# Kernel tuning notes

Measured on AMD Instinct MI355X. Metric: run time of the kernel, lower is better.

## Reference

```python
import jax, jax.numpy as jnp
import numpy as np

N_GENES = 4264
IN_DIM = 1613
N_REL = 4
DIM1, DIM2, DIM3 = 1340, 920, 740
N_DRUGS = 4000
N_EDGES = 100000
N_NODES = N_DRUGS + N_GENES


def setup_inputs() -> dict:
    key = jax.random.key(0)
    ks = jax.random.split(key, 16)
    inp = {}
    inp["x"] = jax.random.normal(ks[0], (N_DRUGS, IN_DIM), dtype=jnp.float32)
    inp["gene_emb"] = jax.random.normal(ks[1], (N_GENES, IN_DIM), dtype=jnp.float32)
    s = 0.02
    inp["w_rel1"] = jax.random.normal(ks[2], (N_REL, IN_DIM, DIM1), dtype=jnp.float32) * s
    inp["root1"] = jax.random.normal(ks[3], (IN_DIM, DIM1), dtype=jnp.float32) * s
    inp["b1"] = jnp.zeros((DIM1,), dtype=jnp.float32)
    inp["w_rel2"] = jax.random.normal(ks[4], (N_REL, DIM1, DIM2), dtype=jnp.float32) * s
    inp["root2"] = jax.random.normal(ks[5], (DIM1, DIM2), dtype=jnp.float32) * s
    inp["b2"] = jnp.zeros((DIM2,), dtype=jnp.float32)
    inp["lin1_w"] = jax.random.normal(ks[6], (DIM2, DIM3), dtype=jnp.float32) * s
    inp["lin1_b"] = jnp.zeros((DIM3,), dtype=jnp.float32)
    inp["lin2_w"] = jax.random.normal(ks[7], (DIM3, 2), dtype=jnp.float32) * s
    inp["lin2_b"] = jnp.zeros((2,), dtype=jnp.float32)
    inp["edge_index"] = jax.random.randint(ks[8], (2, N_EDGES), 0, N_NODES, dtype=jnp.int32)
    inp["edge_type"] = jax.random.randint(ks[9], (N_EDGES,), 0, N_REL, dtype=jnp.int32)
    return inp


def rgcn_conv(x, edge_index, edge_type, w_rel, root, bias):
    # PyG RGCNConv: per-relation linear transform of source node features,
    # scatter-MEAN aggregation per (target node, relation), plus root + bias.
    # Transform-then-gather (N << E) is mathematically identical to gather-then-transform.
    n = x.shape[0]
    r = w_rel.shape[0]
    h = jnp.einsum('nf,rfo->rno', x, w_rel)          # (R, N, out)
    src, dst = edge_index[0], edge_index[1]
    msg = h[edge_type, src]                           # (E, out) gathered messages
    seg = dst * r + edge_type                         # fused (node, relation) segment id
    sums = jax.ops.segment_sum(msg, seg, num_segments=n * r)
    cnts = jax.ops.segment_sum(jnp.ones_like(msg[:, 0]), seg, num_segments=n * r)
    mean = sums / jnp.maximum(cnts, 1.0)[:, None]
    agg = mean.reshape(n, r, -1).sum(axis=1)          # sum over relations
    return agg + x @ root + bias


def reference(x, gene_emb, w_rel1, root1, b1, w_rel2, root2, b2,
              lin1_w, lin1_b, lin2_w, lin2_b, edge_index, edge_type):
    # eval mode: dropout is identity
    xf = jnp.concatenate([x, gene_emb], axis=0)       # (N, 1613)
    h = jax.nn.relu(rgcn_conv(xf, edge_index, edge_type, w_rel1, root1, b1))
    h = jax.nn.relu(rgcn_conv(h, edge_index, edge_type, w_rel2, root2, b2))
    emb = jax.nn.relu(h @ lin1_w + lin1_b)            # (N, 740)
    logits = emb @ lin2_w + lin2_b                    # (N, 2)
    return jax.nn.log_softmax(logits, axis=-1), emb
```

## Files before the change

### kernel.cpp

```cpp
#include <hip/hip_runtime.h>
#include <math.h>

#define N_DRUGS 4000
#define NN      8264
#define IN_DIM  1613
#define NRELS   4
#define DD1     1340
#define DD2     920
#define DD3     740
#define NEDGE   100000
#define NSEG    (NN * NRELS)

#define K1P     1632
#define K2P     1344
#define K3P     928
#define N1PAD   1408
#define N2PAD   1024
#define N3PAD   768
#define MT      65

typedef unsigned short u16;
typedef __attribute__((ext_vector_type(8))) short short8;
typedef __attribute__((ext_vector_type(4))) short short4v;
typedef __attribute__((ext_vector_type(4))) float floatx4;

__device__ __forceinline__ u16 f2bf(float f) {
  union { float f; unsigned u; } v; v.f = f;
  unsigned u = v.u + 0x7fffu + ((v.u >> 16) & 1u);
  return (u16)(u >> 16);
}
__device__ __forceinline__ float bf2f(u16 h) {
  union { unsigned u; float f; } v; v.u = ((unsigned)h) << 16;
  return v.f;
}

__device__ __forceinline__ void gload16(const u16* g, u16* l) {
  __builtin_amdgcn_global_load_lds(
      (const __attribute__((address_space(1))) unsigned int*)g,
      (__attribute__((address_space(3))) unsigned int*)l, 16, 0, 0);
}

__global__ void k_zero_i32(int* p, int n) {
  int i = blockIdx.x * 256 + threadIdx.x;
  if (i < n) p[i] = 0;
}

__global__ void k_zero_u16v(u16* p, long long nvec) {
  long long i = (long long)blockIdx.x * 256 + threadIdx.x;
  if (i < nvec) {
    short8 z = {0,0,0,0,0,0,0,0};
    *((short8*)p + i) = z;
  }
}

__global__ void k_copy_i32(const int* a, int* b, int n) {
  int i = blockIdx.x * 256 + threadIdx.x;
  if (i < n) b[i] = a[i];
}

__global__ void k_hist(const int* __restrict__ ei, const int* __restrict__ et,
                       int* __restrict__ counts) {
  int e = blockIdx.x * 256 + threadIdx.x;
  if (e < NEDGE) {
    int dst = ei[NEDGE + e];
    atomicAdd(&counts[dst * 4 + et[e]], 1);
  }
}

__global__ void k_scan(const int* __restrict__ counts, int* __restrict__ offsets) {
  __shared__ int part[1024];
  int tid = threadIdx.x;
  const int chunk = (NSEG + 1023) / 1024;
  int lo = tid * chunk, hi = min(lo + chunk, NSEG);
  int s = 0;
  for (int i = lo; i < hi; i++) s += counts[i];
  part[tid] = s;
  __syncthreads();
  for (int off = 1; off < 1024; off <<= 1) {
    int v = (tid >= off) ? part[tid - off] : 0;
    __syncthreads();
    part[tid] += v;
    __syncthreads();
  }
  int base = (tid == 0) ? 0 : part[tid - 1];
  for (int i = lo; i < hi; i++) { offsets[i] = base; base += counts[i]; }
  if (tid == 0) offsets[NSEG] = part[1023];
}

__global__ void k_fill(const int* __restrict__ ei, const int* __restrict__ et,
                       int* __restrict__ cursors, int* __restrict__ ssrc) {
  int e = blockIdx.x * 256 + threadIdx.x;
  if (e < NEDGE) {
    int src = ei[e], dst = ei[NEDGE + e];
    int pos = atomicAdd(&cursors[dst * 4 + et[e]], 1);
    if (pos < NEDGE) ssrc[pos] = src;
  }
}

__global__ void k_build_xf(const float* __restrict__ x, const float* __restrict__ gene,
                           u16* __restrict__ xf) {
  int n = blockIdx.x;
  const float* srow = (n < N_DRUGS) ? (x + (long long)n * IN_DIM)
                                    : (gene + (long long)(n - N_DRUGS) * IN_DIM);
  u16* dst = xf + (long long)n * K1P;
  for (int f = threadIdx.x; f < K1P; f += 256)
    dst[f] = (f < IN_DIM) ? f2bf(srow[f]) : (u16)0;
}

__global__ void k_transpose(const float* __restrict__ in, int K, int N,
                            u16* __restrict__ out, int ldd,
                            long long strideIn, long long strideOut) {
  __shared__ float t[32][33];
  const float* inp = in + (long long)blockIdx.z * strideIn;
  u16* outp = out + (long long)blockIdx.z * strideOut;
  int k0 = blockIdx.x * 32, n0 = blockIdx.y * 32;
  int tx = threadIdx.x, ty = threadIdx.y;
  for (int i = ty; i < 32; i += 8) {
    int k = k0 + i, n = n0 + tx;
    t[i][tx] = (k < K && n < N) ? inp[(long long)k * N + n] : 0.f;
  }
  __syncthreads();
  for (int i = ty; i < 32; i += 8) {
    int n = n0 + i, k = k0 + tx;
    if (n < N && k < K) outp[(long long)n * ldd + k] = f2bf(t[tx][i]);
  }
}

__global__ void k_agg2(const u16* __restrict__ T, int ldT, int slotOfs,
                       u16* __restrict__ HACC, int ldH, int F,
                       const int* __restrict__ offsets, const int* __restrict__ ssrc,
                       int rbase, int init) {
  int node = blockIdx.x;
  int s0 = node * 4 + rbase;
  int b0 = offsets[s0],     e0 = offsets[s0 + 1];
  int b1 = offsets[s0 + 1], e1 = offsets[s0 + 2];
  float inv0 = (e0 > b0) ? 1.0f / (float)(e0 - b0) : 0.0f;
  float inv1 = (e1 > b1) ? 1.0f / (float)(e1 - b1) : 0.0f;
  u16* o = HACC + (long long)node * ldH;
  int F8 = F >> 3;
  for (int f8 = threadIdx.x; f8 < F8; f8 += 256) {
    int fo = f8 << 3;
    float a0=0.f,a1=0.f,a2=0.f,a3=0.f,a4=0.f,a5=0.f,a6=0.f,a7=0.f;
    for (int e = b0; e < e0; e++) {
      short8 v = *(const short8*)(T + (long long)ssrc[e] * ldT + fo);
      a0 += bf2f((u16)v[0]); a1 += bf2f((u16)v[1]);
      a2 += bf2f((u16)v[2]); a3 += bf2f((u16)v[3]);
      a4 += bf2f((u16)v[4]); a5 += bf2f((u16)v[5]);
      a6 += bf2f((u16)v[6]); a7 += bf2f((u16)v[7]);
    }
    float c0=0.f,c1=0.f,c2=0.f,c3=0.f,c4=0.f,c5=0.f,c6=0.f,c7=0.f;
    for (int e = b1; e < e1; e++) {
      short8 v = *(const short8*)(T + (long long)ssrc[e] * ldT + slotOfs + fo);
      c0 += bf2f((u16)v[0]); c1 += bf2f((u16)v[1]);
      c2 += bf2f((u16)v[2]); c3 += bf2f((u16)v[3]);
      c4 += bf2f((u16)v[4]); c5 += bf2f((u16)v[5]);
      c6 += bf2f((u16)v[6]); c7 += bf2f((u16)v[7]);
    }
    float r0 = a0*inv0 + c0*inv1, r1 = a1*inv0 + c1*inv1;
    float r2 = a2*inv0 + c2*inv1, r3 = a3*inv0 + c3*inv1;
    float r4 = a4*inv0 + c4*inv1, r5 = a5*inv0 + c5*inv1;
    float r6 = a6*inv0 + c6*inv1, r7 = a7*inv0 + c7*inv1;
    if (!init) {
      short8 pv = *(const short8*)(o + fo);
      r0 += bf2f((u16)pv[0]); r1 += bf2f((u16)pv[1]);
      r2 += bf2f((u16)pv[2]); r3 += bf2f((u16)pv[3]);
      r4 += bf2f((u16)pv[4]); r5 += bf2f((u16)pv[5]);
      r6 += bf2f((u16)pv[6]); r7 += bf2f((u16)pv[7]);
    }
    short8 ov;
    ov[0] = (short)f2bf(r0); ov[1] = (short)f2bf(r1);
    ov[2] = (short)f2bf(r2); ov[3] = (short)f2bf(r3);
    ov[4] = (short)f2bf(r4); ov[5] = (short)f2bf(r5);
    ov[6] = (short)f2bf(r6); ov[7] = (short)f2bf(r7);
    *(short8*)(o + fo) = ov;
  }
  if ((F & 7) && threadIdx.x == 0) {
    for (int f = F & ~7; f < F; f++) {
      float a = 0.f, c = 0.f;
      for (int e = b0; e < e0; e++) a += bf2f(T[(long long)ssrc[e] * ldT + f]);
      for (int e = b1; e < e1; e++) c += bf2f(T[(long long)ssrc[e] * ldT + slotOfs + f]);
      float r = a * inv0 + c * inv1;
      if (!init) r += bf2f(o[f]);
      o[f] = f2bf(r);
    }
  }
}

#define TBUF (128 * 32)

__global__ __launch_bounds__(256)
void k_gemm3(const u16* __restrict__ A, int lda,
             const u16* __restrict__ B, int ldb, int ksteps,
             void* __restrict__ Cout, int ldc,
             const u16* __restrict__ Cacc, int ldacc,
             int nreal, int nlimit, int mlimit,
             const float* __restrict__ bias, int relu, int f32out,
             int mtiles, int ntiles)
{
  int f = blockIdx.x;
  int xr = f & 7, q = f >> 3;
  int Ma = (mtiles + 7) >> 3;
  int ncol = q / Ma;
  int mi = ((q - ncol * Ma) << 3) + xr;
  if (mi >= mtiles) return;

  __shared__ __align__(16) u16 At[3 * TBUF];
  __shared__ __align__(16) u16 Bt[3 * TBUF];
  int tid = threadIdx.x;
  int wave = tid >> 6, lane = tid & 63;
  int wm = (wave >> 1) << 6, wn = (wave & 1) << 6;
  int qd = lane >> 4, l16 = lane & 15;

  const u16* Ag = A + (long long)mi * 128 * lda;
  const u16* Bg = B + (long long)ncol * 128 * ldb;

  int row = tid >> 2, cc = tid & 3;
  int swc = cc ^ ((row >> 1) & 3);
  const u16* gA0 = Ag + (long long)row * lda + swc * 8;
  const u16* gA1 = Ag + (long long)(row + 64) * lda + swc * 8;
  const u16* gB0 = Bg + (long long)row * ldb + swc * 8;
  const u16* gB1 = Bg + (long long)(row + 64) * ldb + swc * 8;
  int d0 = tid * 8;
  int d1 = tid * 8 + 64 * 32;
  int rofs = ((qd ^ ((l16 >> 1) & 3)) << 3);

  unsigned baseA = (unsigned)(unsigned long long)(void*)At;
  unsigned baseB = (unsigned)(unsigned long long)(void*)Bt;
  unsigned offA[4], offB[4];
#pragma unroll
  for (int i = 0; i < 4; i++) {
    offA[i] = (unsigned)(((wm + i * 16 + l16) * 32 + rofs) * 2);
    offB[i] = (unsigned)(((wn + i * 16 + l16) * 32 + rofs) * 2);
  }

  gload16(gA0, At + d0); gload16(gA1, At + d1);
  gload16(gB0, Bt + d0); gload16(gB1, Bt + d1);
  if (ksteps > 1) {
    gload16(gA0 + 32, At + TBUF + d0); gload16(gA1 + 32, At + TBUF + d1);
    gload16(gB0 + 32, Bt + TBUF + d0); gload16(gB1 + 32, Bt + TBUF + d1);
  }

  floatx4 acc[4][4] = {};
  int bs = 0;

  for (int ks = 0; ks < ksteps; ks++) {
    if (ks + 1 < ksteps) asm volatile("s_waitcnt vmcnt(4)" ::: "memory");
    else                 asm volatile("s_waitcnt vmcnt(0)" ::: "memory");
    __builtin_amdgcn_s_barrier();
    __builtin_amdgcn_sched_barrier(0);
    if (ks + 2 < ksteps) {
      int ns = bs + 2; if (ns >= 3) ns -= 3;
      int kb = (ks + 2) * 32;
      u16* An = At + ns * TBUF;
      u16* Bn = Bt + ns * TBUF;
      gload16(gA0 + kb, An + d0); gload16(gA1 + kb, An + d1);
      gload16(gB0 + kb, Bn + d0); gload16(gB1 + kb, Bn + d1);
    }
    unsigned sb = (unsigned)(bs * (TBUF * 2));
    short8 af[4], bfr[4];
#pragma unroll
    for (int i = 0; i < 4; i++)
      asm volatile("ds_read_b128 %0, %1" : "=v"(af[i]) : "v"(baseA + sb + offA[i]));
#pragma unroll
    for (int j = 0; j < 4; j++)
      asm volatile("ds_read_b128 %0, %1" : "=v"(bfr[j]) : "v"(baseB + sb + offB[j]));
    asm volatile("s_waitcnt lgkmcnt(0)" ::: "memory");
    __builtin_amdgcn_sched_barrier(0);
#pragma unroll
    for (int i = 0; i < 4; i++)
#pragma unroll
      for (int j = 0; j < 4; j++)
        acc[i][j] = __builtin_amdgcn_mfma_f32_16x16x32_bf16(af[i], bfr[j], acc[i][j], 0, 0, 0);
    bs++; if (bs >= 3) bs = 0;
  }

#pragma unroll
  for (int i = 0; i < 4; i++) {
#pragma unroll
    for (int j = 0; j < 4; j++) {
      int col = ncol * 128 + wn + j * 16 + l16;
      if (col >= nlimit) continue;
      float bv = (bias && col < nreal) ? bias[col] : 0.f;
#pragma unroll
      for (int rg = 0; rg < 4; rg++) {
        int rowc = mi * 128 + wm + i * 16 + qd * 4 + rg;
        if (rowc >= mlimit) continue;
        float v = 0.f;
        if (col < nreal) {
          v = acc[i][j][rg] + bv;
          if (Cacc) v += bf2f(Cacc[(long long)rowc * ldacc + col]);
          if (relu) v = fmaxf(v, 0.f);
        }
        if (f32out) ((float*)Cout)[(long long)rowc * ldc + col] = v;
        else        ((u16*)Cout)[(long long)rowc * ldc + col] = f2bf(v);
      }
    }
  }
}

__global__ __launch_bounds__(256)
void k_gemm4(const u16* __restrict__ A, int lda,
             const u16* __restrict__ B, int ldb, int ksteps,
             void* __restrict__ Cout, int ldc,
             const u16* __restrict__ Cacc, int ldacc,
             int nreal, int nlimit, int mlimit,
             const float* __restrict__ bias, int relu, int f32out,
             int mtiles, int ntiles)
{
  int f = blockIdx.x;
  int xr = f & 7, q = f >> 3;
  int Ma = (mtiles + 7) >> 3;
  int ncol = q / Ma;
  int mi = ((q - ncol * Ma) << 3) + xr;
  if (mi >= mtiles) return;

  __shared__ __align__(16) u16 At[4 * TBUF];
  __shared__ __align__(16) u16 Bt[4 * TBUF];
  int tid = threadIdx.x;
  int wave = tid >> 6, lane = tid & 63;
  int wm = (wave >> 1) << 6, wn = (wave & 1) << 6;
  int qd = lane >> 4, l16 = lane & 15;

  const u16* Ag = A + (long long)mi * 128 * lda;
  const u16* Bg = B + (long long)ncol * 128 * ldb;

  int row = tid >> 2, cc = tid & 3;
  int swc = cc ^ ((row >> 1) & 3);
  const u16* gA0 = Ag + (long long)row * lda + swc * 8;
  const u16* gA1 = Ag + (long long)(row + 64) * lda + swc * 8;
  const u16* gB0 = Bg + (long long)row * ldb + swc * 8;
  const u16* gB1 = Bg + (long long)(row + 64) * ldb + swc * 8;
  int d0 = tid * 8;
  int d1 = tid * 8 + 64 * 32;
  int rofs = ((qd ^ ((l16 >> 1) & 3)) << 3);

  unsigned baseA = (unsigned)(unsigned long long)(void*)At;
  unsigned baseB = (unsigned)(unsigned long long)(void*)Bt;
  unsigned offA[4], offB[4];
#pragma unroll
  for (int i = 0; i < 4; i++) {
    offA[i] = (unsigned)(((wm + i * 16 + l16) * 32 + rofs) * 2);
    offB[i] = (unsigned)(((wn + i * 16 + l16) * 32 + rofs) * 2);
  }

  gload16(gA0, At + d0); gload16(gA1, At + d1);
  gload16(gB0, Bt + d0); gload16(gB1, Bt + d1);
  if (ksteps > 1) {
    gload16(gA0 + 32, At + TBUF + d0); gload16(gA1 + 32, At + TBUF + d1);
    gload16(gB0 + 32, Bt + TBUF + d0); gload16(gB1 + 32, Bt + TBUF + d1);
  }
  if (ksteps > 2) {
    gload16(gA0 + 64, At + 2 * TBUF + d0); gload16(gA1 + 64, At + 2 * TBUF + d1);
    gload16(gB0 + 64, Bt + 2 * TBUF + d0); gload16(gB1 + 64, Bt + 2 * TBUF + d1);
  }

  floatx4 acc[4][4] = {};
  int bs = 0;

  for (int ks = 0; ks < ksteps; ks++) {
    int rem = ksteps - 1 - ks;
    if (rem >= 2)      asm volatile("s_waitcnt vmcnt(8)" ::: "memory");
    else if (rem == 1) asm volatile("s_waitcnt vmcnt(4)" ::: "memory");
    else               asm volatile("s_waitcnt vmcnt(0)" ::: "memory");
    __builtin_amdgcn_s_barrier();
    __builtin_amdgcn_sched_barrier(0);
    if (ks + 3 < ksteps) {
      int ns = (bs + 3) & 3;
      int kb = (ks + 3) * 32;
      u16* An = At + ns * TBUF;
      u16* Bn = Bt + ns * TBUF;
      gload16(gA0 + kb, An + d0); gload16(gA1 + kb, An + d1);
      gload16(gB0 + kb, Bn + d0); gload16(gB1 + kb, Bn + d1);
    }
    unsigned sb = (unsigned)(bs * (TBUF * 2));
    short8 af[4], bfr[4];
#pragma unroll
    for (int i = 0; i < 4; i++)
      asm volatile("ds_read_b128 %0, %1" : "=v"(af[i]) : "v"(baseA + sb + offA[i]));
#pragma unroll
    for (int j = 0; j < 4; j++)
      asm volatile("ds_read_b128 %0, %1" : "=v"(bfr[j]) : "v"(baseB + sb + offB[j]));
    asm volatile("s_waitcnt lgkmcnt(0)" ::: "memory");
    __builtin_amdgcn_sched_barrier(0);
#pragma unroll
    for (int i = 0; i < 4; i++)
#pragma unroll
      for (int j = 0; j < 4; j++)
        acc[i][j] = __builtin_amdgcn_mfma_f32_16x16x32_bf16(af[i], bfr[j], acc[i][j], 0, 0, 0);
    bs = (bs + 1) & 3;
  }

#pragma unroll
  for (int i = 0; i < 4; i++) {
#pragma unroll
    for (int j = 0; j < 4; j++) {
      int col = ncol * 128 + wn + j * 16 + l16;
      if (col >= nlimit) continue;
      float bv = (bias && col < nreal) ? bias[col] : 0.f;
#pragma unroll
      for (int rg = 0; rg < 4; rg++) {
        int rowc = mi * 128 + wm + i * 16 + qd * 4 + rg;
        if (rowc >= mlimit) continue;
        float v = 0.f;
        if (col < nreal) {
          v = acc[i][j][rg] + bv;
          if (Cacc) v += bf2f(Cacc[(long long)rowc * ldacc + col]);
          if (relu) v = fmaxf(v, 0.f);
        }
        if (f32out) ((float*)Cout)[(long long)rowc * ldc + col] = v;
        else        ((u16*)Cout)[(long long)rowc * ldc + col] = f2bf(v);
      }
    }
  }
}

__global__ void k_lin2(const float* __restrict__ emb, const float* __restrict__ w,
                       const float* __restrict__ b, float* __restrict__ out) {
  int node = blockIdx.x * 4 + (threadIdx.x >> 6);
  int lane = threadIdx.x & 63;
  if (node >= NN) return;
  const float* e = emb + (long long)node * DD3;
  float a0 = 0.f, a1 = 0.f;
  for (int f = lane; f < DD3; f += 64) {
    float v = e[f];
    a0 += v * w[2 * f];
    a1 += v * w[2 * f + 1];
  }
  for (int off = 32; off > 0; off >>= 1) {
    a0 += __shfl_down(a0, off);
    a1 += __shfl_down(a1, off);
  }
  if (lane == 0) {
    a0 += b[0]; a1 += b[1];
    float m = fmaxf(a0, a1);
    float ls = m + logf(expf(a0 - m) + expf(a1 - m));
    out[(long long)node * 2]     = a0 - ls;
    out[(long long)node * 2 + 1] = a1 - ls;
  }
}

extern "C" void kernel_launch(void* const* d_in, const int* in_sizes, int n_in,
                              void* d_out, int out_size, void* d_ws, size_t ws_size,
                              hipStream_t stream)
{
  const float* x      = (const float*)d_in[0];
  const float* gene   = (const float*)d_in[1];
  const float* w_rel1 = (const float*)d_in[2];
  const float* root1  = (const float*)d_in[3];
  const float* b1     = (const float*)d_in[4];
  const float* w_rel2 = (const float*)d_in[5];
  const float* root2  = (const float*)d_in[6];
  const float* b2     = (const float*)d_in[7];
  const float* lin1_w = (const float*)d_in[8];
  const float* lin1_b = (const float*)d_in[9];
  const float* lin2_w = (const float*)d_in[10];
  const float* lin2_b = (const float*)d_in[11];
  const int*   ei     = (const int*)d_in[12];
  const int*   et     = (const int*)d_in[13];
  float* out = (float*)d_out;

  char* ws = (char*)d_ws;
  size_t off = 0;
  auto alloc = [&](size_t bytes) -> void* {
    void* p = ws + off;
    off += (bytes + 255) & ~(size_t)255;
    return p;
  };
  const size_t W1SLOT = (size_t)N1PAD * K1P;
  const size_t W2SLOT = (size_t)N2PAD * K2P;
  u16* XF   = (u16*)alloc((size_t)NN * K1P * 2);
  u16* T    = (u16*)alloc((size_t)NN * 2 * N1PAD * 2);
  u16* HACC = (u16*)alloc((size_t)NN * K2P * 2);
  u16* H1   = (u16*)alloc((size_t)NN * K2P * 2);
  u16* W1P  = (u16*)alloc(2 * W1SLOT * 2);
  u16* W1R  = (u16*)alloc(W1SLOT * 2);
  u16* W2P  = (u16*)alloc(2 * W2SLOT * 2);
  u16* W2R  = (u16*)alloc(W2SLOT * 2);
  u16* W3T  = (u16*)alloc((size_t)N3PAD * K3P * 2);
  int* counts  = (int*)alloc((NSEG + 1) * 4);
  int* offsets = (int*)alloc((NSEG + 1) * 4);
  int* ssrc    = (int*)alloc((size_t)NEDGE * 4);
  u16* H2 = XF;
  float* emb = out + 2 * NN;

  if (off > ws_size) return;

  k_zero_i32<<<(NSEG + 1 + 255) / 256, 256, 0, stream>>>(counts, NSEG + 1);
  k_hist<<<(NEDGE + 255) / 256, 256, 0, stream>>>(ei, et, counts);
  k_scan<<<1, 1024, 0, stream>>>(counts, offsets);
  k_copy_i32<<<(NSEG + 255) / 256, 256, 0, stream>>>(offsets, counts, NSEG);
  k_fill<<<(NEDGE + 255) / 256, 256, 0, stream>>>(ei, et, counts, ssrc);

  long long wtot = 3LL * W1SLOT + 3LL * W2SLOT + (long long)N3PAD * K3P;
  k_zero_u16v<<<(unsigned)((wtot / 8 + 255) / 256), 256, 0, stream>>>(W1P, wtot / 8);
  dim3 tb(32, 8);
  dim3 g_t1((IN_DIM + 31) / 32, (DD1 + 31) / 32, 2);
  dim3 g_t1s((IN_DIM + 31) / 32, (DD1 + 31) / 32, 1);
  dim3 g_t2((DD1 + 31) / 32, (DD2 + 31) / 32, 2);
  dim3 g_t2s((DD1 + 31) / 32, (DD2 + 31) / 32, 1);

  k_build_xf<<<NN, 256, 0, stream>>>(x, gene, XF);

  const int Ma8 = 8 * ((MT + 7) / 8);
  const int gP1 = Ma8 * (2 * N1PAD / 128);
  const int gR1 = Ma8 * (N1PAD / 128);
  const int gP2 = Ma8 * (2 * N2PAD / 128);
  const int gR2 = Ma8 * (N2PAD / 128);
  const int gL3 = Ma8 * (N3PAD / 128);

  k_transpose<<<g_t1, tb, 0, stream>>>(w_rel1, IN_DIM, DD1, W1P, K1P,
                                       (long long)IN_DIM * DD1, (long long)W1SLOT);
  k_gemm4<<<gP1, 256, 0, stream>>>(XF, K1P, W1P, K1P, K1P / 32,
      T, 2 * N1PAD, (const u16*)nullptr, 0, 2 * N1PAD, 2 * N1PAD, NN,
      (const float*)nullptr, 0, 0, MT, 2 * N1PAD / 128);
  k_agg2<<<NN, 256, 0, stream>>>(T, 2 * N1PAD, N1PAD, HACC, K2P, DD1, offsets, ssrc, 0, 1);
  k_transpose<<<g_t1, tb, 0, stream>>>(w_rel1 + 2LL * IN_DIM * DD1, IN_DIM, DD1, W1P, K1P,
                                       (long long)IN_DIM * DD1, (long long)W1SLOT);
  k_gemm3<<<gP1, 256, 0, stream>>>(XF, K1P, W1P, K1P, K1P / 32,
      T, 2 * N1PAD, (const u16*)nullptr, 0, 2 * N1PAD, 2 * N1PAD, NN,
      (const float*)nullptr, 0, 0, MT, 2 * N1PAD / 128);
  k_agg2<<<NN, 256, 0, stream>>>(T, 2 * N1PAD, N1PAD, HACC, K2P, DD1, offsets, ssrc, 2, 0);
  k_transpose<<<g_t1s, tb, 0, stream>>>(root1, IN_DIM, DD1, W1R, K1P, 0, 0);
  k_gemm3<<<gR1, 256, 0, stream>>>(XF, K1P, W1R, K1P, K1P / 32,
      H1, K2P, HACC, K2P, DD1, K2P, NN, b1, 1, 0, MT, N1PAD / 128);

  k_transpose<<<g_t2, tb, 0, stream>>>(w_rel2, DD1, DD2, W2P, K2P,
                                       (long long)DD1 * DD2, (long long)W2SLOT);
  k_gemm3<<<gP2, 256, 0, stream>>>(H1, K2P, W2P, K2P, K2P / 32,
      T, 2 * N2PAD, (const u16*)nullptr, 0, 2 * N2PAD, 2 * N2PAD, NN,
      (const float*)nullptr, 0, 0, MT, 2 * N2PAD / 128);
  k_agg2<<<NN, 256, 0, stream>>>(T, 2 * N2PAD, N2PAD, HACC, K3P, DD2, offsets, ssrc, 0, 1);
  k_transpose<<<g_t2, tb, 0, stream>>>(w_rel2 + 2LL * DD1 * DD2, DD1, DD2, W2P, K2P,
                                       (long long)DD1 * DD2, (long long)W2SLOT);
  k_gemm3<<<gP2, 256, 0, stream>>>(H1, K2P, W2P, K2P, K2P / 32,
      T, 2 * N2PAD, (const u16*)nullptr, 0, 2 * N2PAD, 2 * N2PAD, NN,
      (const float*)nullptr, 0, 0, MT, 2 * N2PAD / 128);
  k_agg2<<<NN, 256, 0, stream>>>(T, 2 * N2PAD, N2PAD, HACC, K3P, DD2, offsets, ssrc, 2, 0);
  k_transpose<<<g_t2s, tb, 0, stream>>>(root2, DD1, DD2, W2R, K2P, 0, 0);
  k_gemm3<<<gR2, 256, 0, stream>>>(H1, K2P, W2R, K2P, K2P / 32,
      H2, K3P, HACC, K3P, DD2, K3P, NN, b2, 1, 0, MT, N2PAD / 128);

  k_transpose<<<dim3((DD2 + 31) / 32, (DD3 + 31) / 32, 1), tb, 0, stream>>>(
      lin1_w, DD2, DD3, W3T, K3P, 0, 0);
  k_gemm3<<<gL3, 256, 0, stream>>>(H2, K3P, W3T, K3P, K3P / 32,
      emb, DD3, (const u16*)nullptr, 0, DD3, DD3, NN, lin1_b, 1, 1, MT, N3PAD / 128);

  k_lin2<<<(NN + 3) / 4, 256, 0, stream>>>(emb, lin2_w, lin2_b, out);
}
```

Measured before the change: 1.001 ms.

## Use wider 128x256 tile GEMM with 512 threads for relation-pair transforms

Replaces the 128x128 four-stage gemm4 and the 128x128 gemm3 calls for the per-relation-pair transforms with a new k_gemmW kernel. It uses 8 waves per block, a 128x256 output tile and a three-stage LDS pipeline, and its epilogue is simplified to a plain bf16 store. The wider tile reuses each A tile across twice as many output columns, which halves A global loads and block count per GEMM. In exchange, LDS use per block grows and there are fewer blocks, which could reduce occupancy or leave CUs idle in the tail.

```diff
diff --git a/kernel.cpp b/kernel.cpp
--- a/kernel.cpp
+++ b/kernel.cpp
@@ -21,7 +21,6 @@
 
 typedef unsigned short u16;
 typedef __attribute__((ext_vector_type(8))) short short8;
-typedef __attribute__((ext_vector_type(4))) short short4v;
 typedef __attribute__((ext_vector_type(4))) float floatx4;
 
 __device__ __forceinline__ u16 f2bf(float f) {
@@ -187,6 +186,8 @@
 }
 
 #define TBUF (128 * 32)
+#define ATBW (128 * 32)
+#define BTBW (256 * 32)
 
 __global__ __launch_bounds__(256)
 void k_gemm3(const u16* __restrict__ A, int lda,
@@ -298,14 +299,12 @@
   }
 }
 
-__global__ __launch_bounds__(256)
-void k_gemm4(const u16* __restrict__ A, int lda,
+__global__ __launch_bounds__(512)
+void k_gemmW(const u16* __restrict__ A, int lda,
              const u16* __restrict__ B, int ldb, int ksteps,
              void* __restrict__ Cout, int ldc,
-             const u16* __restrict__ Cacc, int ldacc,
-             int nreal, int nlimit, int mlimit,
-             const float* __restrict__ bias, int relu, int f32out,
-             int mtiles, int ntiles)
+             int nlimit, int mlimit,
+             int mtiles)
 {
   int f = blockIdx.x;
   int xr = f & 7, q = f >> 3;
@@ -314,26 +313,32 @@
   int mi = ((q - ncol * Ma) << 3) + xr;
   if (mi >= mtiles) return;
 
-  __shared__ __align__(16) u16 At[4 * TBUF];
-  __shared__ __align__(16) u16 Bt[4 * TBUF];
+  __shared__ __align__(16) u16 At[3 * ATBW];
+  __shared__ __align__(16) u16 Bt[3 * BTBW];
   int tid = threadIdx.x;
   int wave = tid >> 6, lane = tid & 63;
-  int wm = (wave >> 1) << 6, wn = (wave & 1) << 6;
+  int wm = (wave >> 2) << 6;
+  int wn = (wave & 3) << 6;
   int qd = lane >> 4, l16 = lane & 15;
 
   const u16* Ag = A + (long long)mi * 128 * lda;
-  const u16* Bg = B + (long long)ncol * 128 * ldb;
-
-  int row = tid >> 2, cc = tid & 3;
-  int swc = cc ^ ((row >> 1) & 3);
-  const u16* gA0 = Ag + (long long)row * lda + swc * 8;
-  const u16* gA1 = Ag + (long long)(row + 64) * lda + swc * 8;
-  const u16* gB0 = Bg + (long long)row * ldb + swc * 8;
-  const u16* gB1 = Bg + (long long)(row + 64) * ldb + swc * 8;
-  int d0 = tid * 8;
-  int d1 = tid * 8 + 64 * 32;
+  const u16* Bg = B + (long long)ncol * 256 * ldb;
+
+  int rowA = tid >> 2, ccA = tid & 3;
+  int swA = ccA ^ ((rowA >> 1) & 3);
+  const u16* gA = Ag + (long long)rowA * lda + swA * 8;
+  int dA = tid * 8;
+
+  int rowB0 = (wave << 5) + (lane >> 2);
+  int rowB1 = rowB0 + 16;
+  int ccB = lane & 3;
+  int swB = ccB ^ ((rowB0 >> 1) & 3);
+  const u16* gB0 = Bg + (long long)rowB0 * ldb + swB * 8;
+  const u16* gB1 = Bg + (long long)rowB1 * ldb + swB * 8;
+  int dB0 = (wave << 10) + lane * 8;
+  int dB1 = dB0 + 512;
+
   int rofs = ((qd ^ ((l16 >> 1) & 3)) << 3);
-
   unsigned baseA = (unsigned)(unsigned long long)(void*)At;
   unsigned baseB = (unsigned)(unsigned long long)(void*)Bt;
   unsigned offA[4], offB[4];
@@ -343,43 +348,37 @@
     offB[i] = (unsigned)(((wn + i * 16 + l16) * 32 + rofs) * 2);
   }
 
-  gload16(gA0, At + d0); gload16(gA1, At + d1);
-  gload16(gB0, Bt + d0); gload16(gB1, Bt + d1);
+  gload16(gA, At + dA);
+  gload16(gB0, Bt + dB0); gload16(gB1, Bt + dB1);
   if (ksteps > 1) {
-    gload16(gA0 + 32, At + TBUF + d0); gload16(gA1 + 32, At + TBUF + d1);
-    gload16(gB0 + 32, Bt + TBUF + d0); gload16(gB1 + 32, Bt + TBUF + d1);
-  }
-  if (ksteps > 2) {
-    gload16(gA0 + 64, At + 2 * TBUF + d0); gload16(gA1 + 64, At + 2 * TBUF + d1);
-    gload16(gB0 + 64, Bt + 2 * TBUF + d0); gload16(gB1 + 64, Bt + 2 * TBUF + d1);
+    gload16(gA + 32, At + ATBW + dA);
+    gload16(gB0 + 32, Bt + BTBW + dB0); gload16(gB1 + 32, Bt + BTBW + dB1);
   }
 
   floatx4 acc[4][4] = {};
   int bs = 0;
 
   for (int ks = 0; ks < ksteps; ks++) {
-    int rem = ksteps - 1 - ks;
-    if (rem >= 2)      asm volatile("s_waitcnt vmcnt(8)" ::: "memory");
-    else if (rem == 1) asm volatile("s_waitcnt vmcnt(4)" ::: "memory");
-    else               asm volatile("s_waitcnt vmcnt(0)" ::: "memory");
+    if (ks + 1 < ksteps) asm volatile("s_waitcnt vmcnt(3)" ::: "memory");
+    else                 asm volatile("s_waitcnt vmcnt(0)" ::: "memory");
     __builtin_amdgcn_s_barrier();
     __builtin_amdgcn_sched_barrier(0);
-    if (ks + 3 < ksteps) {
-      int ns = (bs + 3) & 3;
-      int kb = (ks + 3) * 32;
-      u16* An = At + ns * TBUF;
-      u16* Bn = Bt + ns * TBUF;
-      gload16(gA0 + kb, An + d0); gload16(gA1 + kb, An + d1);
-      gload16(gB0 + kb, Bn + d0); gload16(gB1 + kb, Bn + d1);
-    }
-    unsigned sb = (unsigned)(bs * (TBUF * 2));
+    if (ks + 2 < ksteps) {
+      int ns = bs + 2; if (ns >= 3) ns -= 3;
+      int kb = (ks + 2) * 32;
+      gload16(gA + kb, At + ns * ATBW + dA);
+      gload16(gB0 + kb, Bt + ns * BTBW + dB0);
+      gload16(gB1 + kb, Bt + ns * BTBW + dB1);
+    }
+    unsigned sbA = (unsigned)(bs * (ATBW * 2));
+    unsigned sbB = (unsigned)(bs * (BTBW * 2));
     short8 af[4], bfr[4];
 #pragma unroll
     for (int i = 0; i < 4; i++)
-      asm volatile("ds_read_b128 %0, %1" : "=v"(af[i]) : "v"(baseA + sb + offA[i]));
+      asm volatile("ds_read_b128 %0, %1" : "=v"(af[i]) : "v"(baseA + sbA + offA[i]));
 #pragma unroll
     for (int j = 0; j < 4; j++)
-      asm volatile("ds_read_b128 %0, %1" : "=v"(bfr[j]) : "v"(baseB + sb + offB[j]));
+      asm volatile("ds_read_b128 %0, %1" : "=v"(bfr[j]) : "v"(baseB + sbB + offB[j]));
     asm volatile("s_waitcnt lgkmcnt(0)" ::: "memory");
     __builtin_amdgcn_sched_barrier(0);
 #pragma unroll
@@ -387,28 +386,20 @@
 #pragma unroll
       for (int j = 0; j < 4; j++)
         acc[i][j] = __builtin_amdgcn_mfma_f32_16x16x32_bf16(af[i], bfr[j], acc[i][j], 0, 0, 0);
-    bs = (bs + 1) & 3;
+    bs++; if (bs >= 3) bs = 0;
   }
 
 #pragma unroll
   for (int i = 0; i < 4; i++) {
 #pragma unroll
     for (int j = 0; j < 4; j++) {
-      int col = ncol * 128 + wn + j * 16 + l16;
+      int col = ncol * 256 + wn + j * 16 + l16;
       if (col >= nlimit) continue;
-      float bv = (bias && col < nreal) ? bias[col] : 0.f;
 #pragma unroll
       for (int rg = 0; rg < 4; rg++) {
         int rowc = mi * 128 + wm + i * 16 + qd * 4 + rg;
         if (rowc >= mlimit) continue;
-        float v = 0.f;
-        if (col < nreal) {
-          v = acc[i][j][rg] + bv;
-          if (Cacc) v += bf2f(Cacc[(long long)rowc * ldacc + col]);
-          if (relu) v = fmaxf(v, 0.f);
-        }
-        if (f32out) ((float*)Cout)[(long long)rowc * ldc + col] = v;
-        else        ((u16*)Cout)[(long long)rowc * ldc + col] = f2bf(v);
+        ((u16*)Cout)[(long long)rowc * ldc + col] = f2bf(acc[i][j][rg]);
       }
     }
   }
@@ -502,23 +493,21 @@
   k_build_xf<<<NN, 256, 0, stream>>>(x, gene, XF);
 
   const int Ma8 = 8 * ((MT + 7) / 8);
-  const int gP1 = Ma8 * (2 * N1PAD / 128);
+  const int gP1W = Ma8 * (2 * N1PAD / 256);
+  const int gP2W = Ma8 * (2 * N2PAD / 256);
   const int gR1 = Ma8 * (N1PAD / 128);
-  const int gP2 = Ma8 * (2 * N2PAD / 128);
   const int gR2 = Ma8 * (N2PAD / 128);
   const int gL3 = Ma8 * (N3PAD / 128);
 
   k_transpose<<<g_t1, tb, 0, stream>>>(w_rel1, IN_DIM, DD1, W1P, K1P,
                                        (long long)IN_DIM * DD1, (long long)W1SLOT);
-  k_gemm4<<<gP1, 256, 0, stream>>>(XF, K1P, W1P, K1P, K1P / 32,
-      T, 2 * N1PAD, (const u16*)nullptr, 0, 2 * N1PAD, 2 * N1PAD, NN,
-      (const float*)nullptr, 0, 0, MT, 2 * N1PAD / 128);
+  k_gemmW<<<gP1W, 512, 0, stream>>>(XF, K1P, W1P, K1P, K1P / 32,
+      T, 2 * N1PAD, 2 * N1PAD, NN, MT);
   k_agg2<<<NN, 256, 0, stream>>>(T, 2 * N1PAD, N1PAD, HACC, K2P, DD1, offsets, ssrc, 0, 1);
   k_transpose<<<g_t1, tb, 0, stream>>>(w_rel1 + 2LL * IN_DIM * DD1, IN_DIM, DD1, W1P, K1P,
                                        (long long)IN_DIM * DD1, (long long)W1SLOT);
-  k_gemm3<<<gP1, 256, 0, stream>>>(XF, K1P, W1P, K1P, K1P / 32,
-      T, 2 * N1PAD, (const u16*)nullptr, 0, 2 * N1PAD, 2 * N1PAD, NN,
-      (const float*)nullptr, 0, 0, MT, 2 * N1PAD / 128);
+  k_gemmW<<<gP1W, 512, 0, stream>>>(XF, K1P, W1P, K1P, K1P / 32,
+      T, 2 * N1PAD, 2 * N1PAD, NN, MT);
   k_agg2<<<NN, 256, 0, stream>>>(T, 2 * N1PAD, N1PAD, HACC, K2P, DD1, offsets, ssrc, 2, 0);
   k_transpose<<<g_t1s, tb, 0, stream>>>(root1, IN_DIM, DD1, W1R, K1P, 0, 0);
   k_gemm3<<<gR1, 256, 0, stream>>>(XF, K1P, W1R, K1P, K1P / 32,
@@ -526,15 +515,13 @@
 
   k_transpose<<<g_t2, tb, 0, stream>>>(w_rel2, DD1, DD2, W2P, K2P,
                                        (long long)DD1 * DD2, (long long)W2SLOT);
-  k_gemm3<<<gP2, 256, 0, stream>>>(H1, K2P, W2P, K2P, K2P / 32,
-      T, 2 * N2PAD, (const u16*)nullptr, 0, 2 * N2PAD, 2 * N2PAD, NN,
-      (const float*)nullptr, 0, 0, MT, 2 * N2PAD / 128);
+  k_gemmW<<<gP2W, 512, 0, stream>>>(H1, K2P, W2P, K2P, K2P / 32,
+      T, 2 * N2PAD, 2 * N2PAD, NN, MT);
   k_agg2<<<NN, 256, 0, stream>>>(T, 2 * N2PAD, N2PAD, HACC, K3P, DD2, offsets, ssrc, 0, 1);
   k_transpose<<<g_t2, tb, 0, stream>>>(w_rel2 + 2LL * DD1 * DD2, DD1, DD2, W2P, K2P,
                                        (long long)DD1 * DD2, (long long)W2SLOT);
-  k_gemm3<<<gP2, 256, 0, stream>>>(H1, K2P, W2P, K2P, K2P / 32,
-      T, 2 * N2PAD, (const u16*)nullptr, 0, 2 * N2PAD, 2 * N2PAD, NN,
-      (const float*)nullptr, 0, 0, MT, 2 * N2PAD / 128);
+  k_gemmW<<<gP2W, 512, 0, stream>>>(H1, K2P, W2P, K2P, K2P / 32,
+      T, 2 * N2PAD, 2 * N2PAD, NN, MT);
   k_agg2<<<NN, 256, 0, stream>>>(T, 2 * N2PAD, N2PAD, HACC, K3P, DD2, offsets, ssrc, 2, 0);
   k_transpose<<<g_t2s, tb, 0, stream>>>(root2, DD1, DD2, W2R, K2P, 0, 0);
   k_gemm3<<<gR2, 256, 0, stream>>>(H1, K2P, W2R, K2P, K2P / 32,
```

After: 922.3 us. -7.9%, faster.
